# Kernel tuning notes

Measured on AMD Instinct MI355X. Metric: run time of the kernel, lower is better.

The kernel has to match this reference:

```python
import jax, jax.numpy as jnp
import numpy as np

B, S, D = 1, 2048, 4096
H, KVH, HD = 32, 8, 128
GROUPS = H // KVH  # 4
SCALE = HD ** -0.5
NEG = jnp.finfo(jnp.float32).min


def rotate_half(x):
    x1 = x[..., : x.shape[-1] // 2]
    x2 = x[..., x.shape[-1] // 2:]
    return jnp.concatenate((-x2, x1), axis=-1)


def setup_inputs() -> dict:
    key = jax.random.key(0)
    ks = jax.random.split(key, 8)
    return {
        "hidden_states": jax.random.normal(ks[0], (B, S, D), dtype=jnp.float32),
        "cos": jax.random.uniform(ks[1], (B, S, HD), dtype=jnp.float32),
        "sin": jax.random.uniform(ks[2], (B, S, HD), dtype=jnp.float32),
        "attention_mask": jnp.ones((B, S), dtype=bool),
        "wq": jax.random.normal(ks[3], (D, H * HD), dtype=jnp.float32) * 0.02,
        "wk": jax.random.normal(ks[4], (D, KVH * HD), dtype=jnp.float32) * 0.02,
        "wv": jax.random.normal(ks[5], (D, KVH * HD), dtype=jnp.float32) * 0.02,
        "wo": jax.random.normal(ks[6], (H * HD, D), dtype=jnp.float32) * 0.02,
    }


def reference(hidden_states, cos, sin, attention_mask, wq, wk, wv, wo):
    b, s, _ = hidden_states.shape
    # projections -> (B,S,heads,head_dim)
    q = (hidden_states @ wq).reshape(b, s, H, HD)
    k = (hidden_states @ wk).reshape(b, s, KVH, HD)
    v = (hidden_states @ wv).reshape(b, s, KVH, HD)
    # RoPE (cos/sin unsqueezed at head axis)
    c = cos[:, :, None, :]
    si = sin[:, :, None, :]
    q = q * c + rotate_half(q) * si
    k = k * c + rotate_half(k) * si
    # GQA: repeat kv heads (cache_index=0, max_len==S -> cache write is identity)
    k = jnp.repeat(k, GROUPS, axis=2)
    v = jnp.repeat(v, GROUPS, axis=2)
    # mask: causal AND padding; bias 0 / -inf
    causal = jnp.tril(jnp.ones((s, s), dtype=bool))[None, None]  # (1,1,S,S)
    mask = causal & attention_mask[:, None, None, :]  # (B,1,S,S)
    bias = jnp.where(mask, 0.0, NEG).astype(hidden_states.dtype)
    # scores (B,H,S,S)
    scores = jnp.einsum("bqhd,bkhd->bhqk", q, k) * SCALE + bias
    attn = jax.nn.softmax(scores, axis=-1)
    out = jnp.einsum("bhqk,bkhd->bqhd", attn, v).reshape(b, s, H * HD)
    return out @ wo
```

## Files before the change

kernel.cpp:

```cpp
#include <hip/hip_runtime.h>
#include <hip/hip_bf16.h>

#define SEQ   2048
#define DM    4096
#define NH    32
#define NKVH  8
#define HD    128
#define NQKV  6144
#define KOFF  4096
#define VOFF  5120
#define QLD   5120
#define SCALE 0.08838834764831845f

typedef __attribute__((ext_vector_type(4))) float f32x4;
typedef __attribute__((ext_vector_type(8))) short short8;

__device__ __forceinline__ unsigned short f2bf(float f) {
  union { float f; unsigned int u; } v; v.f = f;
  unsigned int r = v.u + 0x7FFF + ((v.u >> 16) & 1);
  return (unsigned short)(r >> 16);
}
__device__ __forceinline__ float bf2f(unsigned short b) {
  union { unsigned int u; float f; } v; v.u = ((unsigned int)b) << 16;
  return v.f;
}

__device__ __forceinline__ void gld16(const unsigned short* g, unsigned short* l) {
  __builtin_amdgcn_global_load_lds(
      (const __attribute__((address_space(1))) unsigned int*)g,
      (__attribute__((address_space(3))) unsigned int*)l, 16, 0, 0);
}

__global__ __launch_bounds__(256) void prep(const float* __restrict__ hs,
                                            const float* __restrict__ wq,
                                            const float* __restrict__ wk,
                                            const float* __restrict__ wv,
                                            const float* __restrict__ wo,
                                            unsigned short* __restrict__ hsb,
                                            unsigned short* __restrict__ wqkvT,
                                            unsigned short* __restrict__ woT) {
  __shared__ unsigned short t2[64][72];
  const int bxg = blockIdx.x;
  const int tid = threadIdx.x;
  if (bxg < 8192) {
    size_t i = ((size_t)bxg * 256 + tid) * 4;
    float4 v = *(const float4*)(hs + i);
    ushort4 o;
    o.x = f2bf(v.x); o.y = f2bf(v.y); o.z = f2bf(v.z); o.w = f2bf(v.w);
    *(ushort4*)(hsb + i) = o;
    return;
  }
  const int b  = bxg - 8192;
  const int bx = b % 160;
  const int k0 = (b / 160) * 64;
  const float* W; unsigned short* out; int N, n0, row_off;
  if (bx < 64)      { W = wq; out = wqkvT; N = 4096; n0 = bx * 64;        row_off = 0;    }
  else if (bx < 80) { W = wk; out = wqkvT; N = 1024; n0 = (bx - 64) * 64; row_off = 4096; }
  else if (bx < 96) { W = wv; out = wqkvT; N = 1024; n0 = (bx - 80) * 64; row_off = 5120; }
  else              { W = wo; out = woT;   N = 4096; n0 = (bx - 96) * 64; row_off = 0;    }

  const int n  = tid & 63;
  const int q  = tid >> 6;
#pragma unroll
  for (int i = 0; i < 4; ++i) {
    const int kq = (i * 4 + q) * 4;
    float f0 = W[(size_t)(k0 + kq + 0) * N + n0 + n];
    float f1 = W[(size_t)(k0 + kq + 1) * N + n0 + n];
    float f2 = W[(size_t)(k0 + kq + 2) * N + n0 + n];
    float f3 = W[(size_t)(k0 + kq + 3) * N + n0 + n];
    ushort4 u; u.x = f2bf(f0); u.y = f2bf(f1); u.z = f2bf(f2); u.w = f2bf(f3);
    *(ushort4*)&t2[n][kq] = u;
  }
  __syncthreads();

  const int sn = tid >> 3;
  const int c8 = (tid & 7) * 8;
#pragma unroll
  for (int i = 0; i < 2; ++i) {
    const int nn = sn + i * 32;
    short8 v = *(const short8*)&t2[nn][c8];
    *(short8*)&out[(size_t)(row_off + n0 + nn) * DM + k0 + c8] = v;
  }
}

__global__ __launch_bounds__(256) void gemm_bt(const unsigned short* __restrict__ A,
                                               const unsigned short* __restrict__ Bt,
                                               void* __restrict__ C,
                                               unsigned short* __restrict__ vt,
                                               int M, int N, int K, int ldc, int c_fp32) {
  __shared__ unsigned short As[2][128 * 32];
  __shared__ unsigned short Bs[2][128 * 32];
  const int tid  = threadIdx.x;
  const int m0   = blockIdx.y * 128;
  const int n0   = blockIdx.x * 128;
  const int w    = tid >> 6;
  const int lane = tid & 63;
  const int l16  = lane & 15;
  const int quad = lane >> 4;
  const int wr   = (w >> 1) * 64;
  const int wc   = (w & 1) * 64;

  f32x4 acc[4][4];
#pragma unroll
  for (int i = 0; i < 4; ++i)
#pragma unroll
    for (int j = 0; j < 4; ++j) acc[i][j] = (f32x4){0.f, 0.f, 0.f, 0.f};

  const int sr  = lane >> 2;
  const int pb  = lane & 3;
  const int sws = (sr & 3) ^ ((sr >> 2) & 3);
  const int kb  = ((pb ^ sws) << 3);
  const unsigned short* ga0 = A  + (size_t)(m0 + w * 16 + sr) * K + kb;
  const unsigned short* ga1 = A  + (size_t)(m0 + 64 + w * 16 + sr) * K + kb;
  const unsigned short* gb0 = Bt + (size_t)(n0 + w * 16 + sr) * K + kb;
  const unsigned short* gb1 = Bt + (size_t)(n0 + 64 + w * 16 + sr) * K + kb;
  const int lofs0 = (w * 16) * 32;
  const int lofs1 = (64 + w * 16) * 32;

  const int swf  = (l16 & 3) ^ ((l16 >> 2) & 3);
  const int fcol = ((quad ^ swf) << 3);

  gld16(ga0, &As[0][lofs0]);
  gld16(ga1, &As[0][lofs1]);
  gld16(gb0, &Bs[0][lofs0]);
  gld16(gb1, &Bs[0][lofs1]);

  int p = 0;
  for (int k0 = 0; k0 < K; k0 += 32) {
    __syncthreads();
    if (k0 + 32 < K) {
      gld16(ga0 + k0 + 32, &As[p ^ 1][lofs0]);
      gld16(ga1 + k0 + 32, &As[p ^ 1][lofs1]);
      gld16(gb0 + k0 + 32, &Bs[p ^ 1][lofs0]);
      gld16(gb1 + k0 + 32, &Bs[p ^ 1][lofs1]);
    }
    short8 af[4], bfr[4];
#pragma unroll
    for (int mt = 0; mt < 4; ++mt)
      af[mt] = *(const short8*)&As[p][(wr + mt * 16 + l16) * 32 + fcol];
#pragma unroll
    for (int nt = 0; nt < 4; ++nt)
      bfr[nt] = *(const short8*)&Bs[p][(wc + nt * 16 + l16) * 32 + fcol];
#pragma unroll
    for (int mt = 0; mt < 4; ++mt)
#pragma unroll
      for (int nt = 0; nt < 4; ++nt)
        acc[mt][nt] = __builtin_amdgcn_mfma_f32_16x16x32_bf16(af[mt], bfr[nt], acc[mt][nt], 0, 0, 0);
    p ^= 1;
  }

  if (vt && n0 >= VOFF) {
#pragma unroll
    for (int mt = 0; mt < 4; ++mt)
#pragma unroll
      for (int nt = 0; nt < 4; ++nt) {
        int col  = (n0 - VOFF) + wc + nt * 16 + l16;
        int row0 = m0 + wr + mt * 16 + quad * 4;
        ushort4 ov;
        ov.x = f2bf(acc[mt][nt][0]); ov.y = f2bf(acc[mt][nt][1]);
        ov.z = f2bf(acc[mt][nt][2]); ov.w = f2bf(acc[mt][nt][3]);
        *(ushort4*)&vt[(size_t)col * SEQ + row0] = ov;
      }
  } else if (c_fp32) {
    float* Cf = (float*)C;
#pragma unroll
    for (int mt = 0; mt < 4; ++mt)
#pragma unroll
      for (int nt = 0; nt < 4; ++nt) {
        int col = n0 + wc + nt * 16 + l16;
#pragma unroll
        for (int r = 0; r < 4; ++r)
          Cf[(size_t)(m0 + wr + mt * 16 + quad * 4 + r) * ldc + col] = acc[mt][nt][r];
      }
  } else {
    unsigned short* Cb = (unsigned short*)C;
#pragma unroll
    for (int mt = 0; mt < 4; ++mt)
#pragma unroll
      for (int nt = 0; nt < 4; ++nt) {
        int col = n0 + wc + nt * 16 + l16;
#pragma unroll
        for (int r = 0; r < 4; ++r)
          Cb[(size_t)(m0 + wr + mt * 16 + quad * 4 + r) * ldc + col] = f2bf(acc[mt][nt][r]);
      }
  }
}

__global__ __launch_bounds__(256) void rope_k(unsigned short* __restrict__ QKV,
                                              const float* __restrict__ cosb,
                                              const float* __restrict__ sinb) {
  int idx = blockIdx.x * 256 + threadIdx.x;
  int i  = idx & 63;
  int hk = (idx >> 6) & 7;
  int s  = idx >> 9;
  size_t base = (size_t)s * QLD + KOFF + (size_t)hk * 128;
  float q1 = bf2f(QKV[base + i]);
  float q2 = bf2f(QKV[base + i + 64]);
  float c1 = cosb[s * 128 + i],      s1 = sinb[s * 128 + i];
  float c2 = cosb[s * 128 + i + 64], s2 = sinb[s * 128 + i + 64];
  QKV[base + i]      = f2bf(q1 * c1 - q2 * s1);
  QKV[base + i + 64] = f2bf(q2 * c2 + q1 * s2);
}

__global__ __launch_bounds__(256) void flash_attn(const unsigned short* __restrict__ QKV,
                                                  const unsigned short* __restrict__ Vt_g,
                                                  const float* __restrict__ cosb,
                                                  const float* __restrict__ sinb,
                                                  unsigned short* __restrict__ AO) {
  __shared__ unsigned short Ks[64 * 136];
  __shared__ unsigned short Vs[128 * 72];
  __shared__ unsigned short Ps[4][32 * 68];

  const int p    = (int)blockIdx.y * (int)gridDim.x + (int)blockIdx.x;
  const int h    = (p & 7) * 4 + ((p >> 3) & 3);
  const int qt   = ((int)gridDim.y - 1) - (p >> 5);
  const int kvh = h >> 2;
  const int tid  = threadIdx.x;
  const int w    = tid >> 6;
  const int lane = tid & 63;
  const int l16  = lane & 15;
  const int quad = lane >> 4;
  const int q0   = qt * 128;
  const int qrow_w = q0 + w * 32;

  short8 qf[2][4];
#pragma unroll
  for (int ntq = 0; ntq < 2; ++ntq) {
    const int s_row = qrow_w + ntq * 16 + l16;
    const unsigned short* qp = QKV + (size_t)s_row * QLD + h * HD + quad * 8;
#pragma unroll
    for (int ks = 0; ks < 4; ++ks) qf[ntq][ks] = *(const short8*)(qp + ks * 32);
    const float* cb = cosb + (size_t)s_row * 128 + quad * 8;
    const float* sb = sinb + (size_t)s_row * 128 + quad * 8;
#pragma unroll
    for (int ks = 0; ks < 2; ++ks) {
#pragma unroll
      for (int e = 0; e < 8; ++e) {
        int d = ks * 32 + e;
        float f1 = bf2f((unsigned short)qf[ntq][ks][e]);
        float f2 = bf2f((unsigned short)qf[ntq][ks + 2][e]);
        float c1 = cb[d],      s1v = sb[d];
        float c2 = cb[d + 64], s2v = sb[d + 64];
        qf[ntq][ks][e]     = (short)f2bf(f1 * c1 - f2 * s1v);
        qf[ntq][ks + 2][e] = (short)f2bf(f2 * c2 + f1 * s2v);
      }
    }
  }

  f32x4 o[8][2];
#pragma unroll
  for (int i = 0; i < 8; ++i) { o[i][0] = (f32x4){0,0,0,0}; o[i][1] = (f32x4){0,0,0,0}; }
  float m_i[2] = {-3.0e38f, -3.0e38f}, l_i[2] = {0.f, 0.f};

  const int kr = tid >> 2, kcol0 = (tid & 3) * 32;
  const int vr = tid >> 1, vcol0 = (tid & 1) * 32;
  const unsigned short* kbase = QKV + KOFF + (size_t)kvh * HD + kcol0;
  const unsigned short* vbase = Vt_g + ((size_t)kvh * HD + vr) * SEQ + vcol0;

  const int nch = qt * 2 + 2;

  short8 kv[4], vv[4];
#pragma unroll
  for (int u = 0; u < 4; ++u) kv[u] = *(const short8*)(kbase + (size_t)kr * QLD + u * 8);
#pragma unroll
  for (int u = 0; u < 4; ++u) vv[u] = *(const short8*)(vbase + u * 8);

  for (int c = 0; c < nch; ++c) {
    const int kc = c * 64;
    __builtin_amdgcn_s_barrier();
#pragma unroll
    for (int u = 0; u < 4; ++u) *(short8*)&Ks[kr * 136 + kcol0 + u * 8] = kv[u];
#pragma unroll
    for (int u = 0; u < 4; ++u) *(short8*)&Vs[vr * 72 + vcol0 + u * 8] = vv[u];
    if (c + 1 < nch) {
      const int kn = kc + 64;
#pragma unroll
      for (int u = 0; u < 4; ++u) kv[u] = *(const short8*)(kbase + (size_t)(kn + kr) * QLD + u * 8);
#pragma unroll
      for (int u = 0; u < 4; ++u) vv[u] = *(const short8*)(vbase + kn + u * 8);
    }
    asm volatile("s_waitcnt lgkmcnt(0)" ::: "memory");
    __builtin_amdgcn_s_barrier();

    if (kc <= qrow_w + 31) {
      f32x4 st[4][2];
#pragma unroll
      for (int mt = 0; mt < 4; ++mt) { st[mt][0] = (f32x4){0,0,0,0}; st[mt][1] = (f32x4){0,0,0,0}; }
      __builtin_amdgcn_s_setprio(1);
#pragma unroll
      for (int ks = 0; ks < 4; ++ks)
#pragma unroll
        for (int mt = 0; mt < 4; ++mt) {
          short8 ak = *(const short8*)&Ks[(mt * 16 + l16) * 136 + ks * 32 + quad * 8];
          st[mt][0] = __builtin_amdgcn_mfma_f32_16x16x32_bf16(ak, qf[0][ks], st[mt][0], 0, 0, 0);
          st[mt][1] = __builtin_amdgcn_mfma_f32_16x16x32_bf16(ak, qf[1][ks], st[mt][1], 0, 0, 0);
        }
      __builtin_amdgcn_s_setprio(0);

      float sc[4][2][4];
      const bool fullch = (kc + 64 <= qrow_w);
      if (fullch) {
#pragma unroll
        for (int mt = 0; mt < 4; ++mt)
#pragma unroll
          for (int ntq = 0; ntq < 2; ++ntq)
#pragma unroll
            for (int r = 0; r < 4; ++r) sc[mt][ntq][r] = st[mt][ntq][r] * SCALE;
      } else {
#pragma unroll
        for (int mt = 0; mt < 4; ++mt)
#pragma unroll
          for (int ntq = 0; ntq < 2; ++ntq) {
            int qr = qrow_w + ntq * 16 + l16;
#pragma unroll
            for (int r = 0; r < 4; ++r) {
              int key = kc + mt * 16 + quad * 4 + r;
              float v = st[mt][ntq][r] * SCALE;
              sc[mt][ntq][r] = (key <= qr) ? v : -__builtin_inff();
            }
          }
      }
      float mx[2] = {-__builtin_inff(), -__builtin_inff()};
#pragma unroll
      for (int mt = 0; mt < 4; ++mt)
#pragma unroll
        for (int ntq = 0; ntq < 2; ++ntq)
#pragma unroll
          for (int r = 0; r < 4; ++r) mx[ntq] = fmaxf(mx[ntq], sc[mt][ntq][r]);
#pragma unroll
      for (int ntq = 0; ntq < 2; ++ntq) {
        mx[ntq] = fmaxf(mx[ntq], __shfl_xor(mx[ntq], 16, 64));
        mx[ntq] = fmaxf(mx[ntq], __shfl_xor(mx[ntq], 32, 64));
      }

      bool upd = (mx[0] > m_i[0] + 8.f) || (mx[1] > m_i[1] + 8.f);
      if (__any(upd ? 1 : 0)) {
        float al[2];
#pragma unroll
        for (int ntq = 0; ntq < 2; ++ntq) {
          float mn = fmaxf(m_i[ntq], mx[ntq]);
          al[ntq] = __expf(m_i[ntq] - mn);
          m_i[ntq] = mn;
          l_i[ntq] *= al[ntq];
        }
#pragma unroll
        for (int i = 0; i < 8; ++i) {
          o[i][0][0] *= al[0]; o[i][0][1] *= al[0]; o[i][0][2] *= al[0]; o[i][0][3] *= al[0];
          o[i][1][0] *= al[1]; o[i][1][1] *= al[1]; o[i][1][2] *= al[1]; o[i][1][3] *= al[1];
        }
      }

      float rs[2] = {0.f, 0.f};
      unsigned short* psw = &Ps[w][0];
#pragma unroll
      for (int mt = 0; mt < 4; ++mt)
#pragma unroll
        for (int ntq = 0; ntq < 2; ++ntq) {
          float p0 = __expf(sc[mt][ntq][0] - m_i[ntq]);
          float p1 = __expf(sc[mt][ntq][1] - m_i[ntq]);
          float p2 = __expf(sc[mt][ntq][2] - m_i[ntq]);
          float p3 = __expf(sc[mt][ntq][3] - m_i[ntq]);
          rs[ntq] += (p0 + p1) + (p2 + p3);
          ushort4 pk; pk.x = f2bf(p0); pk.y = f2bf(p1); pk.z = f2bf(p2); pk.w = f2bf(p3);
          *(ushort4*)&psw[(ntq * 16 + l16) * 68 + mt * 16 + quad * 4] = pk;
        }
#pragma unroll
      for (int ntq = 0; ntq < 2; ++ntq) {
        rs[ntq] += __shfl_xor(rs[ntq], 16, 64);
        rs[ntq] += __shfl_xor(rs[ntq], 32, 64);
        l_i[ntq] += rs[ntq];
      }

#pragma unroll
      for (int ks = 0; ks < 2; ++ks) {
        short8 bp[2];
#pragma unroll
        for (int ntq = 0; ntq < 2; ++ntq) {
          union { ushort4 h[2]; short8 v; } u;
          const unsigned short* pp = &psw[(ntq * 16 + l16) * 68 + ks * 32 + quad * 8];
          u.h[0] = *(const ushort4*)(pp);
          u.h[1] = *(const ushort4*)(pp + 4);
          bp[ntq] = u.v;
        }
        __builtin_amdgcn_s_setprio(1);
#pragma unroll
        for (int mt = 0; mt < 8; ++mt) {
          short8 av = *(const short8*)&Vs[(mt * 16 + l16) * 72 + ks * 32 + quad * 8];
          o[mt][0] = __builtin_amdgcn_mfma_f32_16x16x32_bf16(av, bp[0], o[mt][0], 0, 0, 0);
          o[mt][1] = __builtin_amdgcn_mfma_f32_16x16x32_bf16(av, bp[1], o[mt][1], 0, 0, 0);
        }
        __builtin_amdgcn_s_setprio(0);
      }
    }
  }

  float inv[2] = {1.0f / l_i[0], 1.0f / l_i[1]};
#pragma unroll
  for (int mt = 0; mt < 8; ++mt)
#pragma unroll
    for (int ntq = 0; ntq < 2; ++ntq) {
      int qr = qrow_w + ntq * 16 + l16;
      int col = h * HD + mt * 16 + quad * 4;
      ushort4 ov;
      ov.x = f2bf(o[mt][ntq][0] * inv[ntq]);
      ov.y = f2bf(o[mt][ntq][1] * inv[ntq]);
      ov.z = f2bf(o[mt][ntq][2] * inv[ntq]);
      ov.w = f2bf(o[mt][ntq][3] * inv[ntq]);
      *(ushort4*)&AO[(size_t)qr * DM + col] = ov;
    }
}

extern "C" void kernel_launch(void* const* d_in, const int* in_sizes, int n_in,
                              void* d_out, int out_size, void* d_ws, size_t ws_size,
                              hipStream_t stream) {
  const float* hs   = (const float*)d_in[0];
  const float* cosb = (const float*)d_in[1];
  const float* sinb = (const float*)d_in[2];
  const float* wq = (const float*)d_in[4];
  const float* wk = (const float*)d_in[5];
  const float* wv = (const float*)d_in[6];
  const float* wo = (const float*)d_in[7];
  float* out = (float*)d_out;

  char* ws = (char*)d_ws;
  unsigned short* hsb   = (unsigned short*)(ws);
  unsigned short* wqkvT = (unsigned short*)(ws + (16u << 20));
  unsigned short* woT   = (unsigned short*)(ws + (64u << 20));
  unsigned short* qkv   = (unsigned short*)(ws + (96u << 20));
  unsigned short* ao    = (unsigned short*)(ws + (116u << 20));
  unsigned short* Vt_g  = (unsigned short*)(ws + (132u << 20));

  prep<<<8192 + 160 * 64, 256, 0, stream>>>(hs, wq, wk, wv, wo, hsb, wqkvT, woT);
  gemm_bt<<<dim3(NQKV / 128, SEQ / 128), 256, 0, stream>>>(hsb, wqkvT, qkv, Vt_g, SEQ, NQKV, DM, QLD, 0);
  rope_k<<<4096, 256, 0, stream>>>(qkv, cosb, sinb);
  flash_attn<<<dim3(NH, SEQ / 128), 256, 0, stream>>>(qkv, Vt_g, cosb, sinb, ao);
  gemm_bt<<<dim3(DM / 128, SEQ / 128), 256, 0, stream>>>(ao, woT, out, nullptr, SEQ, DM, DM, DM, 1);
}
```

Before: 519.9 us.

## Move wo conversion and transpose into the flash attention launch tail

```diff
diff --git a/kernel.cpp b/kernel.cpp
--- a/kernel.cpp
+++ b/kernel.cpp
@@ -35,10 +35,8 @@
                                             const float* __restrict__ wq,
                                             const float* __restrict__ wk,
                                             const float* __restrict__ wv,
-                                            const float* __restrict__ wo,
                                             unsigned short* __restrict__ hsb,
-                                            unsigned short* __restrict__ wqkvT,
-                                            unsigned short* __restrict__ woT) {
+                                            unsigned short* __restrict__ wqkvT) {
   __shared__ unsigned short t2[64][72];
   const int bxg = blockIdx.x;
   const int tid = threadIdx.x;
@@ -51,13 +49,12 @@
     return;
   }
   const int b  = bxg - 8192;
-  const int bx = b % 160;
-  const int k0 = (b / 160) * 64;
-  const float* W; unsigned short* out; int N, n0, row_off;
-  if (bx < 64)      { W = wq; out = wqkvT; N = 4096; n0 = bx * 64;        row_off = 0;    }
-  else if (bx < 80) { W = wk; out = wqkvT; N = 1024; n0 = (bx - 64) * 64; row_off = 4096; }
-  else if (bx < 96) { W = wv; out = wqkvT; N = 1024; n0 = (bx - 80) * 64; row_off = 5120; }
-  else              { W = wo; out = woT;   N = 4096; n0 = (bx - 96) * 64; row_off = 0;    }
+  const int bx = b % 96;
+  const int k0 = (b / 96) * 64;
+  const float* W; int N, n0, row_off;
+  if (bx < 64)      { W = wq; N = 4096; n0 = bx * 64;        row_off = 0;    }
+  else if (bx < 80) { W = wk; N = 1024; n0 = (bx - 64) * 64; row_off = 4096; }
+  else              { W = wv; N = 1024; n0 = (bx - 80) * 64; row_off = 5120; }
 
   const int n  = tid & 63;
   const int q  = tid >> 6;
@@ -79,7 +76,7 @@
   for (int i = 0; i < 2; ++i) {
     const int nn = sn + i * 32;
     short8 v = *(const short8*)&t2[nn][c8];
-    *(short8*)&out[(size_t)(row_off + n0 + nn) * DM + k0 + c8] = v;
+    *(short8*)&wqkvT[(size_t)(row_off + n0 + nn) * DM + k0 + c8] = v;
   }
 }
 
@@ -206,16 +203,48 @@
                                                   const unsigned short* __restrict__ Vt_g,
                                                   const float* __restrict__ cosb,
                                                   const float* __restrict__ sinb,
+                                                  const float* __restrict__ wo,
+                                                  unsigned short* __restrict__ woT,
                                                   unsigned short* __restrict__ AO) {
   __shared__ unsigned short Ks[64 * 136];
   __shared__ unsigned short Vs[128 * 72];
   __shared__ unsigned short Ps[4][32 * 68];
 
-  const int p    = (int)blockIdx.y * (int)gridDim.x + (int)blockIdx.x;
+  const int p   = (int)blockIdx.x;
+  const int tid = threadIdx.x;
+
+  if (p >= 512) {
+    unsigned short (*t2)[72] = (unsigned short (*)[72])Ks;
+    const int b  = p - 512;
+    const int n0 = (b & 63) * 64;
+    const int k0 = (b >> 6) * 64;
+    const int n  = tid & 63;
+    const int q  = tid >> 6;
+#pragma unroll
+    for (int i = 0; i < 4; ++i) {
+      const int kq = (i * 4 + q) * 4;
+      float f0 = wo[(size_t)(k0 + kq + 0) * DM + n0 + n];
+      float f1 = wo[(size_t)(k0 + kq + 1) * DM + n0 + n];
+      float f2 = wo[(size_t)(k0 + kq + 2) * DM + n0 + n];
+      float f3 = wo[(size_t)(k0 + kq + 3) * DM + n0 + n];
+      ushort4 u; u.x = f2bf(f0); u.y = f2bf(f1); u.z = f2bf(f2); u.w = f2bf(f3);
+      *(ushort4*)&t2[n][kq] = u;
+    }
+    __syncthreads();
+    const int sn = tid >> 3;
+    const int c8 = (tid & 7) * 8;
+#pragma unroll
+    for (int i = 0; i < 2; ++i) {
+      const int nn = sn + i * 32;
+      short8 v = *(const short8*)&t2[nn][c8];
+      *(short8*)&woT[(size_t)(n0 + nn) * DM + k0 + c8] = v;
+    }
+    return;
+  }
+
   const int h    = (p & 7) * 4 + ((p >> 3) & 3);
-  const int qt   = ((int)gridDim.y - 1) - (p >> 5);
-  const int kvh = h >> 2;
-  const int tid  = threadIdx.x;
+  const int qt   = (SEQ / 128 - 1) - (p >> 5);
+  const int kvh  = h >> 2;
   const int w    = tid >> 6;
   const int lane = tid & 63;
   const int l16  = lane & 15;
@@ -430,9 +459,9 @@
   unsigned short* ao    = (unsigned short*)(ws + (116u << 20));
   unsigned short* Vt_g  = (unsigned short*)(ws + (132u << 20));
 
-  prep<<<8192 + 160 * 64, 256, 0, stream>>>(hs, wq, wk, wv, wo, hsb, wqkvT, woT);
+  prep<<<8192 + 96 * 64, 256, 0, stream>>>(hs, wq, wk, wv, hsb, wqkvT);
   gemm_bt<<<dim3(NQKV / 128, SEQ / 128), 256, 0, stream>>>(hsb, wqkvT, qkv, Vt_g, SEQ, NQKV, DM, QLD, 0);
   rope_k<<<4096, 256, 0, stream>>>(qkv, cosb, sinb);
-  flash_attn<<<dim3(NH, SEQ / 128), 256, 0, stream>>>(qkv, Vt_g, cosb, sinb, ao);
+  flash_attn<<<512 + 4096, 256, 0, stream>>>(qkv, Vt_g, cosb, sinb, wo, woT, ao);
   gemm_bt<<<dim3(DM / 128, SEQ / 128), 256, 0, stream>>>(ao, woT, out, nullptr, SEQ, DM, DM, DM, 1);
 }
```

New measurement: 510.1 us. About the same (-1.9%).
